# Optimization experiments

Measured on AMD Instinct MI355X. Metric: run time of the kernel, lower is better.

## Reference

```python
import jax, jax.numpy as jnp
import numpy as np

N_NODES = 100000
N_EDGES = 600000
IN_DIM = 128
OUT_DIM = 64


def setup_inputs() -> dict:
    key = jax.random.key(0)
    k1, k2, k3, k4, k5 = jax.random.split(key, 5)
    x = jax.random.normal(k1, (N_NODES, IN_DIM), dtype=jnp.float32)
    edge_index = jax.random.randint(k2, (2, N_EDGES), 0, N_NODES, dtype=jnp.int64)
    edge_weight = jax.random.uniform(k3, (N_EDGES,), dtype=jnp.float32)
    W1 = jax.random.normal(k4, (IN_DIM, IN_DIM), dtype=jnp.float32) / np.sqrt(IN_DIM)
    b1 = jnp.zeros((IN_DIM,), dtype=jnp.float32)
    W2 = jax.random.normal(k5, (IN_DIM, OUT_DIM), dtype=jnp.float32) / np.sqrt(IN_DIM)
    b2 = jnp.zeros((OUT_DIM,), dtype=jnp.float32)
    return {"x": x, "edge_index": edge_index, "edge_weight": edge_weight,
            "W1": W1, "b1": b1, "W2": W2, "b2": b2}


def _spmm(edge_index, edge_weight, h):
    # out[dst] = sum_{e: dst(e)=dst} w_e * h[src(e)]  -- normalized adjacency SpMM
    src, dst = edge_index[0], edge_index[1]
    msg = h[src] * edge_weight[:, None]          # [E, D] gather + scale
    return jax.ops.segment_sum(msg, dst, num_segments=h.shape[0])  # [N, D]


def reference(x, edge_index, edge_weight, W1, b1, W2, b2):
    # Layer 1: GCNConv(in,in) -> ReLU (dropout is identity in eval mode)
    h = _spmm(edge_index, edge_weight, x @ W1) + b1
    h = jax.nn.relu(h)
    # Layer 2: GCNConv(in,out)
    out = _spmm(edge_index, edge_weight, h @ W2) + b2
    return out
```

## Files before the change

kernel.cpp:

```cpp
#include <hip/hip_runtime.h>

#define NN 100000
#define NE 600000
#define DIN 128
#define DOUT 64
#define SCAN_B 512
#define NBLK ((NN + SCAN_B - 1) / SCAN_B)
#define HIST_B ((NE + 255) / 256)
#define PREP_N (DIN * DIN + DIN * DOUT)
#define PREP_B ((PREP_N + 255) / 256)

typedef __attribute__((ext_vector_type(8))) short bf16x8;
typedef __attribute__((ext_vector_type(4))) short s16x4;
typedef __attribute__((ext_vector_type(4))) float f32x4;
typedef __attribute__((ext_vector_type(2))) float f32x2;

__device__ inline short f2bf(float f) {
  union { float f; unsigned u; } v; v.f = f;
  unsigned r = (v.u + 0x7FFF + ((v.u >> 16) & 1)) >> 16;
  return (short)r;
}
__device__ inline float bf2f(unsigned short u) {
  union { unsigned u; float f; } v; v.u = ((unsigned)u) << 16;
  return v.f;
}
__device__ inline unsigned char f2fp8(float f) {
  unsigned pk = __builtin_amdgcn_cvt_pk_fp8_f32(f, f, 0, false);
  return (unsigned char)(pk & 0xff);
}
__device__ inline void fma_fp8x16(uint4 q, float w, float* acc) {
  f32x2 f;
  f = __builtin_amdgcn_cvt_pk_f32_fp8(q.x, false); acc[0] += w * f[0];  acc[1] += w * f[1];
  f = __builtin_amdgcn_cvt_pk_f32_fp8(q.x, true);  acc[2] += w * f[0];  acc[3] += w * f[1];
  f = __builtin_amdgcn_cvt_pk_f32_fp8(q.y, false); acc[4] += w * f[0];  acc[5] += w * f[1];
  f = __builtin_amdgcn_cvt_pk_f32_fp8(q.y, true);  acc[6] += w * f[0];  acc[7] += w * f[1];
  f = __builtin_amdgcn_cvt_pk_f32_fp8(q.z, false); acc[8] += w * f[0];  acc[9] += w * f[1];
  f = __builtin_amdgcn_cvt_pk_f32_fp8(q.z, true);  acc[10] += w * f[0]; acc[11] += w * f[1];
  f = __builtin_amdgcn_cvt_pk_f32_fp8(q.w, false); acc[12] += w * f[0]; acc[13] += w * f[1];
  f = __builtin_amdgcn_cvt_pk_f32_fp8(q.w, true);  acc[14] += w * f[0]; acc[15] += w * f[1];
}

__global__ __launch_bounds__(256) void hist_prep_kernel(const int* __restrict__ ei,
                                                        int* __restrict__ cnt,
                                                        int* __restrict__ rank,
                                                        const float* __restrict__ W1,
                                                        short* __restrict__ w1t,
                                                        const float* __restrict__ W2,
                                                        short* __restrict__ w2t) {
  const int b = blockIdx.x, t = threadIdx.x;
  if (b < HIST_B) {
    int e = b * 256 + t;
    if (e < NE) rank[e] = atomicAdd(&cnt[ei[NE + e]], 1);
  } else {
    int i = (b - HIST_B) * 256 + t;
    if (i < DIN * DIN) {
      int n = i >> 7, k = i & 127;
      w1t[i] = f2bf(W1[k * DIN + n]);
    } else if (i < PREP_N) {
      int i2 = i - DIN * DIN;
      int n = i2 >> 7, k = i2 & 127;
      w2t[i2] = f2bf(W2[k * DOUT + n]);
    }
  }
}

__global__ __launch_bounds__(512) void scan_local_kernel(const int* __restrict__ cnt,
                                                         int* __restrict__ row_ptr,
                                                         int* __restrict__ blk_sum) {
  __shared__ int s[512];
  const int b = blockIdx.x, t = threadIdx.x;
  const int i = b * 512 + t;
  int v = (i < NN) ? cnt[i] : 0;
  s[t] = v;
  __syncthreads();
  for (int off = 1; off < 512; off <<= 1) {
    int u = (t >= off) ? s[t - off] : 0;
    __syncthreads();
    s[t] += u;
    __syncthreads();
  }
  if (i < NN) row_ptr[i] = s[t] - v;
  if (t == 511) blk_sum[b] = s[511];
}

__global__ __launch_bounds__(512) void scan_add_kernel(int* __restrict__ row_ptr,
                                                       const int* __restrict__ blk_sum) {
  __shared__ int s[512];
  const int b = blockIdx.x, t = threadIdx.x;
  s[t] = (t < NBLK) ? blk_sum[t] : 0;
  __syncthreads();
  for (int off = 1; off < 512; off <<= 1) {
    int u = (t >= off) ? s[t - off] : 0;
    __syncthreads();
    s[t] += u;
    __syncthreads();
  }
  int off = (b > 0) ? s[b - 1] : 0;
  const int i = b * 512 + t;
  if (i < NN) row_ptr[i] += off;
  if (b == 0 && t == 0) row_ptr[NN] = NE;
}

__global__ __launch_bounds__(256) void scatter_kernel(const int* __restrict__ ei,
                                                      const float* __restrict__ ew,
                                                      const int* __restrict__ row_ptr,
                                                      const int* __restrict__ rank,
                                                      int2* __restrict__ ep) {
  int e = blockIdx.x * 256 + threadIdx.x;
  if (e >= NE) return;
  int src = ei[e];
  int dst = ei[NE + e];
  int pos = row_ptr[dst] + rank[e];
  ep[pos] = make_int2(src, __float_as_int(ew[e]));
}

#define G1_BM 128
#define XS_PITCH 136
__global__ __launch_bounds__(256) void gemm1_mfma_kernel(const float* __restrict__ x,
                                                         const short* __restrict__ w1t,
                                                         unsigned char* __restrict__ h0) {
  __shared__ short xs[G1_BM][XS_PITCH];
  const int t = threadIdx.x;
  const int row0 = blockIdx.x * G1_BM;
#pragma unroll
  for (int i = 0; i < 16; ++i) {
    int f = t + i * 256;
    int r = f >> 5, c4 = f & 31;
    int gr = row0 + r;
    float4 v = (gr < NN) ? *(const float4*)&x[(size_t)gr * DIN + c4 * 4]
                         : make_float4(0.f, 0.f, 0.f, 0.f);
    s16x4 s;
    s.x = f2bf(v.x); s.y = f2bf(v.y); s.z = f2bf(v.z); s.w = f2bf(v.w);
    *(s16x4*)&xs[r][c4 * 4] = s;
  }
  __syncthreads();

  const int wave = t >> 6, lane = t & 63;
  const int nlane = lane & 15, quad = lane >> 4;
  const int mbase = wave * 32;
  f32x4 acc[2][8];
#pragma unroll
  for (int mt = 0; mt < 2; ++mt)
#pragma unroll
    for (int nt = 0; nt < 8; ++nt) acc[mt][nt] = (f32x4){0.f, 0.f, 0.f, 0.f};

#pragma unroll
  for (int ks = 0; ks < 4; ++ks) {
    const int koff = ks * 32 + quad * 8;
    bf16x8 a0 = *(const bf16x8*)&xs[mbase + nlane][koff];
    bf16x8 a1 = *(const bf16x8*)&xs[mbase + 16 + nlane][koff];
#pragma unroll
    for (int nt = 0; nt < 8; ++nt) {
      bf16x8 b = *(const bf16x8*)&w1t[(size_t)(nt * 16 + nlane) * DIN + koff];
      acc[0][nt] = __builtin_amdgcn_mfma_f32_16x16x32_bf16(a0, b, acc[0][nt], 0, 0, 0);
      acc[1][nt] = __builtin_amdgcn_mfma_f32_16x16x32_bf16(a1, b, acc[1][nt], 0, 0, 0);
    }
  }

#pragma unroll
  for (int mt = 0; mt < 2; ++mt)
#pragma unroll
    for (int nt = 0; nt < 8; ++nt)
#pragma unroll
      for (int rg = 0; rg < 4; ++rg) {
        int gr = row0 + mbase + mt * 16 + quad * 4 + rg;
        if (gr < NN) h0[(size_t)gr * DIN + nt * 16 + nlane] = f2fp8(acc[mt][nt][rg]);
      }
}

__global__ __launch_bounds__(256) void gemm2_mfma_kernel(const short* __restrict__ acc1,
                                                         const float* __restrict__ b1,
                                                         const short* __restrict__ w2t,
                                                         short* __restrict__ h2) {
  __shared__ short xs[G1_BM][XS_PITCH];
  const int t = threadIdx.x;
  const int row0 = blockIdx.x * G1_BM;
#pragma unroll
  for (int i = 0; i < 8; ++i) {
    int f = t + i * 256;
    int r = f >> 4, c8 = f & 15;
    int gr = row0 + r;
    bf16x8 v = (gr < NN) ? *(const bf16x8*)&acc1[(size_t)gr * DIN + c8 * 8]
                         : (bf16x8){0, 0, 0, 0, 0, 0, 0, 0};
    bf16x8 s;
#pragma unroll
    for (int j = 0; j < 8; ++j) {
      float fv = bf2f((unsigned short)v[j]) + b1[c8 * 8 + j];
      s[j] = f2bf(fmaxf(fv, 0.f));
    }
    *(bf16x8*)&xs[r][c8 * 8] = s;
  }
  __syncthreads();

  const int wave = t >> 6, lane = t & 63;
  const int nlane = lane & 15, quad = lane >> 4;
  const int mbase = wave * 32;
  f32x4 acc[2][4];
#pragma unroll
  for (int mt = 0; mt < 2; ++mt)
#pragma unroll
    for (int nt = 0; nt < 4; ++nt) acc[mt][nt] = (f32x4){0.f, 0.f, 0.f, 0.f};

#pragma unroll
  for (int ks = 0; ks < 4; ++ks) {
    const int koff = ks * 32 + quad * 8;
    bf16x8 a0 = *(const bf16x8*)&xs[mbase + nlane][koff];
    bf16x8 a1 = *(const bf16x8*)&xs[mbase + 16 + nlane][koff];
#pragma unroll
    for (int nt = 0; nt < 4; ++nt) {
      bf16x8 b = *(const bf16x8*)&w2t[(size_t)(nt * 16 + nlane) * DIN + koff];
      acc[0][nt] = __builtin_amdgcn_mfma_f32_16x16x32_bf16(a0, b, acc[0][nt], 0, 0, 0);
      acc[1][nt] = __builtin_amdgcn_mfma_f32_16x16x32_bf16(a1, b, acc[1][nt], 0, 0, 0);
    }
  }

#pragma unroll
  for (int mt = 0; mt < 2; ++mt)
#pragma unroll
    for (int nt = 0; nt < 4; ++nt)
#pragma unroll
      for (int rg = 0; rg < 4; ++rg) {
        int gr = row0 + mbase + mt * 16 + quad * 4 + rg;
        if (gr < NN) h2[(size_t)gr * DOUT + nt * 16 + nlane] = f2bf(acc[mt][nt][rg]);
      }
}

__global__ __launch_bounds__(256) void spmm1_fp8_kernel(const int* __restrict__ rp,
                                                        const int2* __restrict__ ep,
                                                        const unsigned char* __restrict__ h,
                                                        short* __restrict__ acc1) {
  const int row = blockIdx.x * 32 + (threadIdx.x >> 3);
  const int lane = threadIdx.x & 7;
  if (row >= NN) return;
  const int b = rp[row], e = rp[row + 1];
  float acc[16];
#pragma unroll
  for (int j = 0; j < 16; ++j) acc[j] = 0.f;
  int i = b;
  for (; i + 4 <= e; i += 4) {
    int2 p0 = ep[i], p1 = ep[i + 1], p2 = ep[i + 2], p3 = ep[i + 3];
    uint4 q0 = *(const uint4*)&h[(size_t)p0.x * DIN + lane * 16];
    uint4 q1 = *(const uint4*)&h[(size_t)p1.x * DIN + lane * 16];
    uint4 q2 = *(const uint4*)&h[(size_t)p2.x * DIN + lane * 16];
    uint4 q3 = *(const uint4*)&h[(size_t)p3.x * DIN + lane * 16];
    fma_fp8x16(q0, __int_as_float(p0.y), acc);
    fma_fp8x16(q1, __int_as_float(p1.y), acc);
    fma_fp8x16(q2, __int_as_float(p2.y), acc);
    fma_fp8x16(q3, __int_as_float(p3.y), acc);
  }
  if (i + 2 <= e) {
    int2 p0 = ep[i], p1 = ep[i + 1];
    uint4 q0 = *(const uint4*)&h[(size_t)p0.x * DIN + lane * 16];
    uint4 q1 = *(const uint4*)&h[(size_t)p1.x * DIN + lane * 16];
    fma_fp8x16(q0, __int_as_float(p0.y), acc);
    fma_fp8x16(q1, __int_as_float(p1.y), acc);
    i += 2;
  }
  if (i < e) {
    int2 p0 = ep[i];
    uint4 q0 = *(const uint4*)&h[(size_t)p0.x * DIN + lane * 16];
    fma_fp8x16(q0, __int_as_float(p0.y), acc);
  }
  bf16x8 o0, o1;
#pragma unroll
  for (int j = 0; j < 8; ++j) { o0[j] = f2bf(acc[j]); o1[j] = f2bf(acc[8 + j]); }
  *(bf16x8*)&acc1[(size_t)row * DIN + lane * 16] = o0;
  *(bf16x8*)&acc1[(size_t)row * DIN + lane * 16 + 8] = o1;
}

__global__ __launch_bounds__(256) void spmm2_kernel(const int* __restrict__ rp,
                                                    const int2* __restrict__ ep,
                                                    const short* __restrict__ h,
                                                    const float* __restrict__ bias,
                                                    float* __restrict__ out) {
  const int row = blockIdx.x * 32 + (threadIdx.x >> 3);
  const int lane = threadIdx.x & 7;
  if (row >= NN) return;
  const int b = rp[row], e = rp[row + 1];
  float acc[8];
#pragma unroll
  for (int j = 0; j < 8; ++j) acc[j] = 0.f;
  int i = b;
  for (; i + 4 <= e; i += 4) {
    int2 p0 = ep[i], p1 = ep[i + 1], p2 = ep[i + 2], p3 = ep[i + 3];
    bf16x8 v0 = *(const bf16x8*)&h[(size_t)p0.x * DOUT + lane * 8];
    bf16x8 v1 = *(const bf16x8*)&h[(size_t)p1.x * DOUT + lane * 8];
    bf16x8 v2 = *(const bf16x8*)&h[(size_t)p2.x * DOUT + lane * 8];
    bf16x8 v3 = *(const bf16x8*)&h[(size_t)p3.x * DOUT + lane * 8];
    float w0 = __int_as_float(p0.y), w1 = __int_as_float(p1.y);
    float w2 = __int_as_float(p2.y), w3 = __int_as_float(p3.y);
#pragma unroll
    for (int j = 0; j < 8; ++j)
      acc[j] += w0 * bf2f((unsigned short)v0[j]) + w1 * bf2f((unsigned short)v1[j]) +
                w2 * bf2f((unsigned short)v2[j]) + w3 * bf2f((unsigned short)v3[j]);
  }
  if (i + 2 <= e) {
    int2 p0 = ep[i], p1 = ep[i + 1];
    bf16x8 v0 = *(const bf16x8*)&h[(size_t)p0.x * DOUT + lane * 8];
    bf16x8 v1 = *(const bf16x8*)&h[(size_t)p1.x * DOUT + lane * 8];
    float w0 = __int_as_float(p0.y), w1 = __int_as_float(p1.y);
#pragma unroll
    for (int j = 0; j < 8; ++j)
      acc[j] += w0 * bf2f((unsigned short)v0[j]) + w1 * bf2f((unsigned short)v1[j]);
    i += 2;
  }
  if (i < e) {
    int2 p0 = ep[i];
    bf16x8 v0 = *(const bf16x8*)&h[(size_t)p0.x * DOUT + lane * 8];
    float w0 = __int_as_float(p0.y);
#pragma unroll
    for (int j = 0; j < 8; ++j) acc[j] += w0 * bf2f((unsigned short)v0[j]);
  }
#pragma unroll
  for (int j = 0; j < 8; ++j) acc[j] += bias[lane * 8 + j];
  *(float4*)&out[(size_t)row * DOUT + lane * 8] = make_float4(acc[0], acc[1], acc[2], acc[3]);
  *(float4*)&out[(size_t)row * DOUT + lane * 8 + 4] = make_float4(acc[4], acc[5], acc[6], acc[7]);
}

extern "C" void kernel_launch(void* const* d_in, const int* in_sizes, int n_in,
                              void* d_out, int out_size, void* d_ws, size_t ws_size,
                              hipStream_t stream) {
  const float* x  = (const float*)d_in[0];
  const int*   ei = (const int*)d_in[1];
  const float* ew = (const float*)d_in[2];
  const float* W1 = (const float*)d_in[3];
  const float* b1 = (const float*)d_in[4];
  const float* W2 = (const float*)d_in[5];
  const float* b2 = (const float*)d_in[6];
  float* out = (float*)d_out;

  char* p = (char*)d_ws;
  int*   cnt     = (int*)p;                 p += sizeof(int) * NN;
  int*   row_ptr = (int*)p;                 p += sizeof(int) * (NN + 4);
  int*   blk_sum = (int*)p;                 p += sizeof(int) * (NBLK + 4);
  int*   rank    = (int*)p;                 p += sizeof(int) * NE;
  int2*  ep      = (int2*)p;                p += sizeof(int2) * NE;
  short* w1t     = (short*)p;               p += sizeof(short) * DIN * DIN;
  short* w2t     = (short*)p;               p += sizeof(short) * DIN * DOUT;
  unsigned char* h0 = (unsigned char*)p;    p += (size_t)NN * DIN;
  short* acc1    = (short*)p;
  short* h2      = (short*)h0;

  hipMemsetAsync(cnt, 0, sizeof(int) * NN, stream);
  hist_prep_kernel<<<HIST_B + PREP_B, 256, 0, stream>>>(ei, cnt, rank, W1, w1t, W2, w2t);
  scan_local_kernel<<<NBLK, 512, 0, stream>>>(cnt, row_ptr, blk_sum);
  scan_add_kernel<<<NBLK, 512, 0, stream>>>(row_ptr, blk_sum);
  scatter_kernel<<<HIST_B, 256, 0, stream>>>(ei, ew, row_ptr, rank, ep);

  gemm1_mfma_kernel<<<(NN + G1_BM - 1) / G1_BM, 256, 0, stream>>>(x, w1t, h0);
  spmm1_fp8_kernel<<<(NN + 31) / 32, 256, 0, stream>>>(row_ptr, ep, h0, acc1);

  gemm2_mfma_kernel<<<(NN + G1_BM - 1) / G1_BM, 256, 0, stream>>>(acc1, b1, w2t, h2);
  spmm2_kernel<<<(NN + 31) / 32, 256, 0, stream>>>(row_ptr, ep, h2, b2, out);
}
```

Before: 236.8 us.

## Fuse SpMM1 with bias/ReLU/GEMM2 and merge histogram with GEMM1

The layer-1 SpMM result is now kept in shared memory and passed directly to the GEMM2 MFMA within one 512-thread block. This removes the bf16 acc1 intermediate write and read and one kernel launch. The edge histogram is merged into the GEMM1 launch, and the memset and weight prep are folded into one prep kernel. GEMM1 now loads x directly from global memory into registers instead of staging it through LDS. The fused SpMM+GEMM2 kernel launches far fewer blocks, each doing more serial work, which may reduce latency hiding during the gathers.

```diff
diff --git a/kernel.cpp b/kernel.cpp
--- a/kernel.cpp
+++ b/kernel.cpp
@@ -7,8 +7,12 @@
 #define SCAN_B 512
 #define NBLK ((NN + SCAN_B - 1) / SCAN_B)
 #define HIST_B ((NE + 255) / 256)
-#define PREP_N (DIN * DIN + DIN * DOUT)
-#define PREP_B ((PREP_N + 255) / 256)
+#define G1_BM 128
+#define G1B ((NN + G1_BM - 1) / G1_BM)
+#define ZB ((NN + 255) / 256)
+#define W1B (DIN * DIN / 256)
+#define W2B (DIN * DOUT / 256)
+#define XS_PITCH 136
 
 typedef __attribute__((ext_vector_type(8))) short bf16x8;
 typedef __attribute__((ext_vector_type(4))) short s16x4;
@@ -27,6 +31,12 @@
 __device__ inline unsigned char f2fp8(float f) {
   unsigned pk = __builtin_amdgcn_cvt_pk_fp8_f32(f, f, 0, false);
   return (unsigned char)(pk & 0xff);
+}
+__device__ inline bf16x8 pack8(float4 u0, float4 u1) {
+  bf16x8 r;
+  r[0] = f2bf(u0.x); r[1] = f2bf(u0.y); r[2] = f2bf(u0.z); r[3] = f2bf(u0.w);
+  r[4] = f2bf(u1.x); r[5] = f2bf(u1.y); r[6] = f2bf(u1.z); r[7] = f2bf(u1.w);
+  return r;
 }
 __device__ inline void fma_fp8x16(uint4 q, float w, float* acc) {
   f32x2 f;
@@ -40,28 +50,81 @@
   f = __builtin_amdgcn_cvt_pk_f32_fp8(q.w, true);  acc[14] += w * f[0]; acc[15] += w * f[1];
 }
 
-__global__ __launch_bounds__(256) void hist_prep_kernel(const int* __restrict__ ei,
-                                                        int* __restrict__ cnt,
-                                                        int* __restrict__ rank,
-                                                        const float* __restrict__ W1,
-                                                        short* __restrict__ w1t,
-                                                        const float* __restrict__ W2,
-                                                        short* __restrict__ w2t) {
+__global__ __launch_bounds__(256) void prep_kernel(int* __restrict__ cnt,
+                                                   const float* __restrict__ W1,
+                                                   short* __restrict__ w1t,
+                                                   const float* __restrict__ W2,
+                                                   short* __restrict__ w2t) {
   const int b = blockIdx.x, t = threadIdx.x;
-  if (b < HIST_B) {
-    int e = b * 256 + t;
+  if (b < ZB) {
+    int i = b * 256 + t;
+    if (i < NN) cnt[i] = 0;
+  } else if (b < ZB + W1B) {
+    int i = (b - ZB) * 256 + t;
+    int n = i >> 7, k = i & 127;
+    w1t[i] = f2bf(W1[k * DIN + n]);
+  } else {
+    int i = (b - ZB - W1B) * 256 + t;
+    int n = i >> 7, k = i & 127;
+    w2t[i] = f2bf(W2[k * DOUT + n]);
+  }
+}
+
+__global__ __launch_bounds__(256) void hist_gemm1_kernel(const int* __restrict__ ei,
+                                                         int* __restrict__ cnt,
+                                                         int* __restrict__ rank,
+                                                         const float* __restrict__ x,
+                                                         const short* __restrict__ w1t,
+                                                         unsigned char* __restrict__ h0) {
+  const int b = blockIdx.x, t = threadIdx.x;
+  if (b >= G1B) {
+    int e = (b - G1B) * 256 + t;
     if (e < NE) rank[e] = atomicAdd(&cnt[ei[NE + e]], 1);
-  } else {
-    int i = (b - HIST_B) * 256 + t;
-    if (i < DIN * DIN) {
-      int n = i >> 7, k = i & 127;
-      w1t[i] = f2bf(W1[k * DIN + n]);
-    } else if (i < PREP_N) {
-      int i2 = i - DIN * DIN;
-      int n = i2 >> 7, k = i2 & 127;
-      w2t[i2] = f2bf(W2[k * DOUT + n]);
-    }
-  }
+    return;
+  }
+  const int row0 = b * G1_BM;
+  const int wave = t >> 6, lane = t & 63;
+  const int nlane = lane & 15, quad = lane >> 4;
+  const int mbase = wave * 32;
+  f32x4 acc[2][8];
+#pragma unroll
+  for (int mt = 0; mt < 2; ++mt)
+#pragma unroll
+    for (int nt = 0; nt < 8; ++nt) acc[mt][nt] = (f32x4){0.f, 0.f, 0.f, 0.f};
+
+  const int ra0 = row0 + mbase + nlane;
+  const int ra1 = ra0 + 16;
+#pragma unroll
+  for (int ks = 0; ks < 4; ++ks) {
+    const int koff = ks * 32 + quad * 8;
+    bf16x8 a0 = (bf16x8){0, 0, 0, 0, 0, 0, 0, 0};
+    bf16x8 a1 = (bf16x8){0, 0, 0, 0, 0, 0, 0, 0};
+    if (ra0 < NN) {
+      float4 u0 = *(const float4*)&x[(size_t)ra0 * DIN + koff];
+      float4 u1 = *(const float4*)&x[(size_t)ra0 * DIN + koff + 4];
+      a0 = pack8(u0, u1);
+    }
+    if (ra1 < NN) {
+      float4 u0 = *(const float4*)&x[(size_t)ra1 * DIN + koff];
+      float4 u1 = *(const float4*)&x[(size_t)ra1 * DIN + koff + 4];
+      a1 = pack8(u0, u1);
+    }
+#pragma unroll
+    for (int nt = 0; nt < 8; ++nt) {
+      bf16x8 bfr = *(const bf16x8*)&w1t[(size_t)(nt * 16 + nlane) * DIN + koff];
+      acc[0][nt] = __builtin_amdgcn_mfma_f32_16x16x32_bf16(a0, bfr, acc[0][nt], 0, 0, 0);
+      acc[1][nt] = __builtin_amdgcn_mfma_f32_16x16x32_bf16(a1, bfr, acc[1][nt], 0, 0, 0);
+    }
+  }
+#pragma unroll
+  for (int mt = 0; mt < 2; ++mt)
+#pragma unroll
+    for (int nt = 0; nt < 8; ++nt)
+#pragma unroll
+      for (int rg = 0; rg < 4; ++rg) {
+        int gr = row0 + mbase + mt * 16 + quad * 4 + rg;
+        if (gr < NN) h0[(size_t)gr * DIN + nt * 16 + nlane] = f2fp8(acc[mt][nt][rg]);
+      }
 }
 
 __global__ __launch_bounds__(512) void scan_local_kernel(const int* __restrict__ cnt,
@@ -114,158 +177,91 @@
   ep[pos] = make_int2(src, __float_as_int(ew[e]));
 }
 
-#define G1_BM 128
-#define XS_PITCH 136
-__global__ __launch_bounds__(256) void gemm1_mfma_kernel(const float* __restrict__ x,
-                                                         const short* __restrict__ w1t,
-                                                         unsigned char* __restrict__ h0) {
+__global__ __launch_bounds__(512) void spmm1_gemm2_kernel(const int* __restrict__ rp,
+                                                          const int2* __restrict__ ep,
+                                                          const unsigned char* __restrict__ h,
+                                                          const float* __restrict__ b1,
+                                                          const short* __restrict__ w2t,
+                                                          short* __restrict__ h2) {
   __shared__ short xs[G1_BM][XS_PITCH];
   const int t = threadIdx.x;
   const int row0 = blockIdx.x * G1_BM;
-#pragma unroll
-  for (int i = 0; i < 16; ++i) {
-    int f = t + i * 256;
-    int r = f >> 5, c4 = f & 31;
-    int gr = row0 + r;
-    float4 v = (gr < NN) ? *(const float4*)&x[(size_t)gr * DIN + c4 * 4]
-                         : make_float4(0.f, 0.f, 0.f, 0.f);
-    s16x4 s;
-    s.x = f2bf(v.x); s.y = f2bf(v.y); s.z = f2bf(v.z); s.w = f2bf(v.w);
-    *(s16x4*)&xs[r][c4 * 4] = s;
+  const int sub = t >> 3, lane8 = t & 7;
+  float bb[16];
+  *(float4*)&bb[0]  = *(const float4*)&b1[lane8 * 16];
+  *(float4*)&bb[4]  = *(const float4*)&b1[lane8 * 16 + 4];
+  *(float4*)&bb[8]  = *(const float4*)&b1[lane8 * 16 + 8];
+  *(float4*)&bb[12] = *(const float4*)&b1[lane8 * 16 + 12];
+
+#pragma unroll
+  for (int batch = 0; batch < 2; ++batch) {
+    const int r = batch * 64 + sub;
+    const int row = row0 + r;
+    float acc[16];
+#pragma unroll
+    for (int j = 0; j < 16; ++j) acc[j] = 0.f;
+    if (row < NN) {
+      const int b0 = rp[row], e1 = rp[row + 1];
+      int i = b0;
+      for (; i + 4 <= e1; i += 4) {
+        int2 p0 = ep[i], p1 = ep[i + 1], p2 = ep[i + 2], p3 = ep[i + 3];
+        uint4 q0 = *(const uint4*)&h[(size_t)p0.x * DIN + lane8 * 16];
+        uint4 q1 = *(const uint4*)&h[(size_t)p1.x * DIN + lane8 * 16];
+        uint4 q2 = *(const uint4*)&h[(size_t)p2.x * DIN + lane8 * 16];
+        uint4 q3 = *(const uint4*)&h[(size_t)p3.x * DIN + lane8 * 16];
+        fma_fp8x16(q0, __int_as_float(p0.y), acc);
+        fma_fp8x16(q1, __int_as_float(p1.y), acc);
+        fma_fp8x16(q2, __int_as_float(p2.y), acc);
+        fma_fp8x16(q3, __int_as_float(p3.y), acc);
+      }
+      if (i + 2 <= e1) {
+        int2 p0 = ep[i], p1 = ep[i + 1];
+        uint4 q0 = *(const uint4*)&h[(size_t)p0.x * DIN + lane8 * 16];
+        uint4 q1 = *(const uint4*)&h[(size_t)p1.x * DIN + lane8 * 16];
+        fma_fp8x16(q0, __int_as_float(p0.y), acc);
+        fma_fp8x16(q1, __int_as_float(p1.y), acc);
+        i += 2;
+      }
+      if (i < e1) {
+        int2 p0 = ep[i];
+        uint4 q0 = *(const uint4*)&h[(size_t)p0.x * DIN + lane8 * 16];
+        fma_fp8x16(q0, __int_as_float(p0.y), acc);
+      }
+    }
+    bf16x8 o0, o1;
+#pragma unroll
+    for (int j = 0; j < 8; ++j) {
+      o0[j] = f2bf(fmaxf(acc[j] + bb[j], 0.f));
+      o1[j] = f2bf(fmaxf(acc[8 + j] + bb[8 + j], 0.f));
+    }
+    *(bf16x8*)&xs[r][lane8 * 16] = o0;
+    *(bf16x8*)&xs[r][lane8 * 16 + 8] = o1;
   }
   __syncthreads();
 
   const int wave = t >> 6, lane = t & 63;
   const int nlane = lane & 15, quad = lane >> 4;
-  const int mbase = wave * 32;
-  f32x4 acc[2][8];
-#pragma unroll
-  for (int mt = 0; mt < 2; ++mt)
-#pragma unroll
-    for (int nt = 0; nt < 8; ++nt) acc[mt][nt] = (f32x4){0.f, 0.f, 0.f, 0.f};
-
+  const int mbase = wave * 16;
+  f32x4 acc2[4];
+#pragma unroll
+  for (int nt = 0; nt < 4; ++nt) acc2[nt] = (f32x4){0.f, 0.f, 0.f, 0.f};
 #pragma unroll
   for (int ks = 0; ks < 4; ++ks) {
     const int koff = ks * 32 + quad * 8;
     bf16x8 a0 = *(const bf16x8*)&xs[mbase + nlane][koff];
-    bf16x8 a1 = *(const bf16x8*)&xs[mbase + 16 + nlane][koff];
-#pragma unroll
-    for (int nt = 0; nt < 8; ++nt) {
-      bf16x8 b = *(const bf16x8*)&w1t[(size_t)(nt * 16 + nlane) * DIN + koff];
-      acc[0][nt] = __builtin_amdgcn_mfma_f32_16x16x32_bf16(a0, b, acc[0][nt], 0, 0, 0);
-      acc[1][nt] = __builtin_amdgcn_mfma_f32_16x16x32_bf16(a1, b, acc[1][nt], 0, 0, 0);
-    }
-  }
-
-#pragma unroll
-  for (int mt = 0; mt < 2; ++mt)
-#pragma unroll
-    for (int nt = 0; nt < 8; ++nt)
-#pragma unroll
-      for (int rg = 0; rg < 4; ++rg) {
-        int gr = row0 + mbase + mt * 16 + quad * 4 + rg;
-        if (gr < NN) h0[(size_t)gr * DIN + nt * 16 + nlane] = f2fp8(acc[mt][nt][rg]);
-      }
-}
-
-__global__ __launch_bounds__(256) void gemm2_mfma_kernel(const short* __restrict__ acc1,
-                                                         const float* __restrict__ b1,
-                                                         const short* __restrict__ w2t,
-                                                         short* __restrict__ h2) {
-  __shared__ short xs[G1_BM][XS_PITCH];
-  const int t = threadIdx.x;
-  const int row0 = blockIdx.x * G1_BM;
-#pragma unroll
-  for (int i = 0; i < 8; ++i) {
-    int f = t + i * 256;
-    int r = f >> 4, c8 = f & 15;
-    int gr = row0 + r;
-    bf16x8 v = (gr < NN) ? *(const bf16x8*)&acc1[(size_t)gr * DIN + c8 * 8]
-                         : (bf16x8){0, 0, 0, 0, 0, 0, 0, 0};
-    bf16x8 s;
-#pragma unroll
-    for (int j = 0; j < 8; ++j) {
-      float fv = bf2f((unsigned short)v[j]) + b1[c8 * 8 + j];
-      s[j] = f2bf(fmaxf(fv, 0.f));
-    }
-    *(bf16x8*)&xs[r][c8 * 8] = s;
-  }
-  __syncthreads();
-
-  const int wave = t >> 6, lane = t & 63;
-  const int nlane = lane & 15, quad = lane >> 4;
-  const int mbase = wave * 32;
-  f32x4 acc[2][4];
-#pragma unroll
-  for (int mt = 0; mt < 2; ++mt)
-#pragma unroll
-    for (int nt = 0; nt < 4; ++nt) acc[mt][nt] = (f32x4){0.f, 0.f, 0.f, 0.f};
-
-#pragma unroll
-  for (int ks = 0; ks < 4; ++ks) {
-    const int koff = ks * 32 + quad * 8;
-    bf16x8 a0 = *(const bf16x8*)&xs[mbase + nlane][koff];
-    bf16x8 a1 = *(const bf16x8*)&xs[mbase + 16 + nlane][koff];
 #pragma unroll
     for (int nt = 0; nt < 4; ++nt) {
-      bf16x8 b = *(const bf16x8*)&w2t[(size_t)(nt * 16 + nlane) * DIN + koff];
-      acc[0][nt] = __builtin_amdgcn_mfma_f32_16x16x32_bf16(a0, b, acc[0][nt], 0, 0, 0);
-      acc[1][nt] = __builtin_amdgcn_mfma_f32_16x16x32_bf16(a1, b, acc[1][nt], 0, 0, 0);
-    }
-  }
-
-#pragma unroll
-  for (int mt = 0; mt < 2; ++mt)
-#pragma unroll
-    for (int nt = 0; nt < 4; ++nt)
-#pragma unroll
-      for (int rg = 0; rg < 4; ++rg) {
-        int gr = row0 + mbase + mt * 16 + quad * 4 + rg;
-        if (gr < NN) h2[(size_t)gr * DOUT + nt * 16 + nlane] = f2bf(acc[mt][nt][rg]);
-      }
-}
-
-__global__ __launch_bounds__(256) void spmm1_fp8_kernel(const int* __restrict__ rp,
-                                                        const int2* __restrict__ ep,
-                                                        const unsigned char* __restrict__ h,
-                                                        short* __restrict__ acc1) {
-  const int row = blockIdx.x * 32 + (threadIdx.x >> 3);
-  const int lane = threadIdx.x & 7;
-  if (row >= NN) return;
-  const int b = rp[row], e = rp[row + 1];
-  float acc[16];
-#pragma unroll
-  for (int j = 0; j < 16; ++j) acc[j] = 0.f;
-  int i = b;
-  for (; i + 4 <= e; i += 4) {
-    int2 p0 = ep[i], p1 = ep[i + 1], p2 = ep[i + 2], p3 = ep[i + 3];
-    uint4 q0 = *(const uint4*)&h[(size_t)p0.x * DIN + lane * 16];
-    uint4 q1 = *(const uint4*)&h[(size_t)p1.x * DIN + lane * 16];
-    uint4 q2 = *(const uint4*)&h[(size_t)p2.x * DIN + lane * 16];
-    uint4 q3 = *(const uint4*)&h[(size_t)p3.x * DIN + lane * 16];
-    fma_fp8x16(q0, __int_as_float(p0.y), acc);
-    fma_fp8x16(q1, __int_as_float(p1.y), acc);
-    fma_fp8x16(q2, __int_as_float(p2.y), acc);
-    fma_fp8x16(q3, __int_as_float(p3.y), acc);
-  }
-  if (i + 2 <= e) {
-    int2 p0 = ep[i], p1 = ep[i + 1];
-    uint4 q0 = *(const uint4*)&h[(size_t)p0.x * DIN + lane * 16];
-    uint4 q1 = *(const uint4*)&h[(size_t)p1.x * DIN + lane * 16];
-    fma_fp8x16(q0, __int_as_float(p0.y), acc);
-    fma_fp8x16(q1, __int_as_float(p1.y), acc);
-    i += 2;
-  }
-  if (i < e) {
-    int2 p0 = ep[i];
-    uint4 q0 = *(const uint4*)&h[(size_t)p0.x * DIN + lane * 16];
-    fma_fp8x16(q0, __int_as_float(p0.y), acc);
-  }
-  bf16x8 o0, o1;
-#pragma unroll
-  for (int j = 0; j < 8; ++j) { o0[j] = f2bf(acc[j]); o1[j] = f2bf(acc[8 + j]); }
-  *(bf16x8*)&acc1[(size_t)row * DIN + lane * 16] = o0;
-  *(bf16x8*)&acc1[(size_t)row * DIN + lane * 16 + 8] = o1;
+      bf16x8 bfr = *(const bf16x8*)&w2t[(size_t)(nt * 16 + nlane) * DIN + koff];
+      acc2[nt] = __builtin_amdgcn_mfma_f32_16x16x32_bf16(a0, bfr, acc2[nt], 0, 0, 0);
+    }
+  }
+#pragma unroll
+  for (int nt = 0; nt < 4; ++nt)
+#pragma unroll
+    for (int rg = 0; rg < 4; ++rg) {
+      int gr = row0 + mbase + quad * 4 + rg;
+      if (gr < NN) h2[(size_t)gr * DOUT + nt * 16 + nlane] = f2bf(acc2[nt][rg]);
+    }
 }
 
 __global__ __launch_bounds__(256) void spmm2_kernel(const int* __restrict__ rp,
@@ -338,18 +334,13 @@
   short* w1t     = (short*)p;               p += sizeof(short) * DIN * DIN;
   short* w2t     = (short*)p;               p += sizeof(short) * DIN * DOUT;
   unsigned char* h0 = (unsigned char*)p;    p += (size_t)NN * DIN;
-  short* acc1    = (short*)p;
-  short* h2      = (short*)h0;
-
-  hipMemsetAsync(cnt, 0, sizeof(int) * NN, stream);
-  hist_prep_kernel<<<HIST_B + PREP_B, 256, 0, stream>>>(ei, cnt, rank, W1, w1t, W2, w2t);
+  short* h2      = (short*)p;
+
+  prep_kernel<<<ZB + W1B + W2B, 256, 0, stream>>>(cnt, W1, w1t, W2, w2t);
+  hist_gemm1_kernel<<<G1B + HIST_B, 256, 0, stream>>>(ei, cnt, rank, x, w1t, h0);
   scan_local_kernel<<<NBLK, 512, 0, stream>>>(cnt, row_ptr, blk_sum);
   scan_add_kernel<<<NBLK, 512, 0, stream>>>(row_ptr, blk_sum);
   scatter_kernel<<<HIST_B, 256, 0, stream>>>(ei, ew, row_ptr, rank, ep);
-
-  gemm1_mfma_kernel<<<(NN + G1_BM - 1) / G1_BM, 256, 0, stream>>>(x, w1t, h0);
-  spmm1_fp8_kernel<<<(NN + 31) / 32, 256, 0, stream>>>(row_ptr, ep, h0, acc1);
-
-  gemm2_mfma_kernel<<<(NN + G1_BM - 1) / G1_BM, 256, 0, stream>>>(acc1, b1, w2t, h2);
+  spmm1_gemm2_kernel<<<G1B, 512, 0, stream>>>(row_ptr, ep, h0, b1, w2t, h2);
   spmm2_kernel<<<(NN + 31) / 32, 256, 0, stream>>>(row_ptr, ep, h2, b2, out);
 }
```

Result: faster. 225.7 us (-4.7%).
